# Kernel optimization log

Measured on AMD Instinct MI355X. Metric: run time of the kernel, lower is better.

The kernel has to match this reference:

```python
import jax, jax.numpy as jnp
import numpy as np

N_HEADS = 16


def setup_inputs() -> dict:
    key = jax.random.key(0)
    ks = jax.random.split(key, 6)
    B, S, E = 2, 2048, 1024
    scale = 1.0 / np.sqrt(E)
    return {
        "X": jax.random.normal(ks[0], (B, S, E), dtype=jnp.float32),
        "Wq": jax.random.normal(ks[1], (E, E), dtype=jnp.float32) * scale,
        "Wk": jax.random.normal(ks[2], (E, E), dtype=jnp.float32) * scale,
        "Wv": jax.random.normal(ks[3], (E, E), dtype=jnp.float32) * scale,
        "Wp": jax.random.normal(ks[4], (E, E), dtype=jnp.float32) * scale,
        "bp": jnp.zeros((E,), dtype=jnp.float32),
    }


def reference(X, Wq, Wk, Wv, Wp, bp):
    B, S, E = X.shape
    H = N_HEADS
    dk = E // H
    # qkv projections (Linear with weight [out,in] -> x @ W.T), split heads
    q = (X @ Wq.T).reshape(B, S, H, dk).transpose(0, 2, 1, 3)  # [B,H,S,dk]
    k = (X @ Wk.T).reshape(B, S, H, dk).transpose(0, 2, 1, 3)
    v = (X @ Wv.T).reshape(B, S, H, dk).transpose(0, 2, 1, 3)
    scores = jnp.einsum('bhqd,bhkd->bhqk', q, k) / jnp.sqrt(jnp.asarray(dk, X.dtype))
    causal = jnp.tril(jnp.ones((S, S), dtype=bool))  # [S,S]
    scores = jnp.where(causal[None, None], scores, jnp.asarray(-jnp.inf, X.dtype))
    attn = jax.nn.softmax(scores, axis=-1)  # [B,H,S,S]
    y = jnp.einsum('bhqk,bhkd->bhqd', attn, v)  # [B,H,S,dk]
    y = y.transpose(0, 2, 1, 3).reshape(B, S, E)
    return y @ Wp.T + bp
```

## Files before the change

### kernel.cpp

```cpp
#include <hip/hip_runtime.h>

typedef unsigned short u16;
typedef __bf16 bf16x8 __attribute__((ext_vector_type(8)));
typedef float f32x4 __attribute__((ext_vector_type(4)));
typedef unsigned short u16x8 __attribute__((ext_vector_type(8)));
typedef unsigned short u16x4 __attribute__((ext_vector_type(4)));

union B8 { u16x8 u; bf16x8 b; };

#define MFMA_BF16(a, b, c) __builtin_amdgcn_mfma_f32_16x16x32_bf16((a), (b), (c), 0, 0, 0)

__device__ __forceinline__ u16 f2bf(float f) {
  unsigned x = __float_as_uint(f);
  unsigned r = x + 0x7fffu + ((x >> 16) & 1u);
  return (u16)(r >> 16);
}

__device__ __forceinline__ unsigned cvt_pk_bf16(float lo, float hi) {
  unsigned r;
  asm("v_cvt_pk_bf16_f32 %0, %1, %2" : "=v"(r) : "v"(lo), "v"(hi));
  return r;
}

__device__ __forceinline__ void gl2lds16(const void* g, void* l) {
  __builtin_amdgcn_global_load_lds(
      (const __attribute__((address_space(1))) void*)g,
      (__attribute__((address_space(3))) void*)l, 16, 0, 0);
}

__global__ __launch_bounds__(256) void cast5_kernel(
    const float* __restrict__ X, const float* __restrict__ Wq,
    const float* __restrict__ Wk, const float* __restrict__ Wv,
    const float* __restrict__ Wp, u16* __restrict__ Xb, u16* __restrict__ Wqb,
    u16* __restrict__ Wkb, u16* __restrict__ Wvb, u16* __restrict__ Wpb) {
  size_t i = ((size_t)blockIdx.x * 256 + threadIdx.x) * 4;
  const float* src;
  u16* dst;
  size_t off;
  if (i < 4194304) {
    src = X; dst = Xb; off = i;
  } else if (i < 5242880) {
    src = Wq; dst = Wqb; off = i - 4194304;
  } else if (i < 6291456) {
    src = Wk; dst = Wkb; off = i - 5242880;
  } else if (i < 7340032) {
    src = Wv; dst = Wvb; off = i - 6291456;
  } else {
    src = Wp; dst = Wpb; off = i - 7340032;
  }
  float4 v = *(const float4*)(src + off);
  u16x4 o;
  o[0] = f2bf(v.x); o[1] = f2bf(v.y); o[2] = f2bf(v.z); o[3] = f2bf(v.w);
  *(u16x4*)(dst + off) = o;
}

template <int MLO>
__device__ __forceinline__ void mfma12(f32x4 (&acc)[8][3], B8 (&af)[8], B8& b0,
                                       B8& b1, B8& b2) {
  __builtin_amdgcn_s_setprio(1);
#pragma unroll
  for (int m = MLO; m < MLO + 4; ++m) {
    acc[m][0] = MFMA_BF16(af[m].b, b0.b, acc[m][0]);
    acc[m][1] = MFMA_BF16(af[m].b, b1.b, acc[m][1]);
    acc[m][2] = MFMA_BF16(af[m].b, b2.b, acc[m][2]);
  }
  __builtin_amdgcn_s_setprio(0);
}

__global__ __launch_bounds__(512, 1) void gemm_qkv192(
    const u16* __restrict__ Xb, const u16* __restrict__ Wb,
    u16* __restrict__ Qb, u16* __restrict__ Kb, u16* __restrict__ Vt) {
  __shared__ __align__(16) u16 Al[2][2][256 * 32];
  __shared__ __align__(16) u16 Bl[2][2][192 * 32];

  int tid = threadIdx.x, lane = tid & 63, w = tid >> 6;
  int wr = w >> 2, wc = w & 3;
  int l16 = lane & 15, lg = lane >> 4;

  int bid = blockIdx.x;
  int swz = (bid & 7) * 32 + (bid >> 3);
  int bm = swz >> 4, bn = swz & 15;

  const u16* Ag = Xb + (size_t)bm * 256 * 1024;
  const u16* Bg = Wb + (size_t)bn * 192 * 1024;

  int lr = lane >> 2;
  int lc = lane & 3;

  auto stA = [&](int buf, int kh, int kt) {
#pragma unroll
    for (int p2 = 0; p2 < 2; ++p2) {
      int r = p2 * 128 + w * 16 + lr;
      int sl = lc ^ ((r >> 1) & 3);
      gl2lds16(Ag + (size_t)r * 1024 + kt * 64 + kh * 32 + sl * 8,
               (char*)&Al[buf][kh][0] + (size_t)(p2 * 128 + w * 16) * 64);
    }
  };
  auto stB = [&](int buf, int kh, int kt) {
    {
      int r = w * 16 + lr;
      int sl = lc ^ ((r >> 1) & 3);
      gl2lds16(Bg + (size_t)r * 1024 + kt * 64 + kh * 32 + sl * 8,
               (char*)&Bl[buf][kh][0] + (size_t)(w * 16) * 64);
    }
    if (w < 4) {
      int r = 128 + w * 16 + lr;
      int sl = lc ^ ((r >> 1) & 3);
      gl2lds16(Bg + (size_t)r * 1024 + kt * 64 + kh * 32 + sl * 8,
               (char*)&Bl[buf][kh][0] + (size_t)(128 + w * 16) * 64);
    }
  };
  auto ldA = [&](int buf, int kk, B8 (&af)[8]) {
#pragma unroll
    for (int m = 0; m < 8; ++m) {
      int r = wr * 128 + m * 16 + l16;
      af[m].u = *(const u16x8*)((const char*)&Al[buf][kk][0] + r * 64 +
                                ((lg ^ ((r >> 1) & 3)) << 4));
    }
  };
  auto ldB = [&](int buf, int kk, int nf, B8& bf) {
    int r = wc * 48 + nf * 16 + l16;
    bf.u = *(const u16x8*)((const char*)&Bl[buf][kk][0] + r * 64 +
                           ((lg ^ ((r >> 1) & 3)) << 4));
  };

#define WAITC(LAST)                                                            \
  do {                                                                         \
    if (LAST) asm volatile("s_waitcnt vmcnt(0)" ::: "memory");                 \
    else if (w < 4) asm volatile("s_waitcnt vmcnt(8)" ::: "memory");           \
    else asm volatile("s_waitcnt vmcnt(6)" ::: "memory");                      \
  } while (0)

  f32x4 acc[8][3] = {};

  stA(0, 0, 0); stB(0, 0, 0);
  stA(0, 1, 0); stB(0, 1, 0);
  stA(1, 0, 1); stB(1, 0, 1);
  WAITC(false);
  __builtin_amdgcn_s_barrier();

  B8 af[8], b0, b1, b2;
  for (int I = 0; I < 8; ++I) {
    int p = 2 * I;
    bool last = (I == 7);
    stA(1, 1, p + 1);
    ldA(0, 0, af); ldB(0, 0, 0, b0); ldB(0, 0, 1, b1); ldB(0, 0, 2, b2);
    mfma12<0>(acc, af, b0, b1, b2);
    stB(1, 1, p + 1);
    mfma12<4>(acc, af, b0, b1, b2);
    WAITC(last);
    __builtin_amdgcn_s_barrier();
    if (!last) stA(0, 0, p + 2);
    ldA(0, 1, af); ldB(0, 1, 0, b0); ldB(0, 1, 1, b1); ldB(0, 1, 2, b2);
    mfma12<0>(acc, af, b0, b1, b2);
    if (!last) stB(0, 0, p + 2);
    mfma12<4>(acc, af, b0, b1, b2);
    WAITC(last);
    __builtin_amdgcn_s_barrier();
    if (!last) stA(0, 1, p + 2);
    ldA(1, 0, af); ldB(1, 0, 0, b0); ldB(1, 0, 1, b1); ldB(1, 0, 2, b2);
    mfma12<0>(acc, af, b0, b1, b2);
    if (!last) stB(0, 1, p + 2);
    mfma12<4>(acc, af, b0, b1, b2);
    WAITC(last);
    __builtin_amdgcn_s_barrier();
    if (!last) stA(1, 0, p + 3);
    ldA(1, 1, af); ldB(1, 1, 0, b0); ldB(1, 1, 1, b1); ldB(1, 1, 2, b2);
    mfma12<0>(acc, af, b0, b1, b2);
    if (!last) stB(1, 0, p + 3);
    mfma12<4>(acc, af, b0, b1, b2);
    if (!last) {
      WAITC(false);
      __builtin_amdgcn_s_barrier();
    }
  }
#undef WAITC

  const float QSCALE = 0.18033688011112042f;
#pragma unroll
  for (int m = 0; m < 8; ++m)
#pragma unroll
    for (int nf = 0; nf < 3; ++nf) {
      int colg = bn * 192 + wc * 48 + nf * 16 + l16;
      int rowg = bm * 256 + wr * 128 + m * 16 + lg * 4;
      if (colg < 1024) {
#pragma unroll
        for (int j = 0; j < 4; ++j)
          Qb[(size_t)(rowg + j) * 1024 + colg] = f2bf(acc[m][nf][j] * QSCALE);
      } else if (colg < 2048) {
#pragma unroll
        for (int j = 0; j < 4; ++j)
          Kb[(size_t)(rowg + j) * 1024 + (colg - 1024)] = f2bf(acc[m][nf][j]);
      } else {
        int cv = colg - 2048;
        int hh = cv >> 6, d = cv & 63;
        int bb = rowg >> 11, s0r = rowg & 2047;
        u16x4 pk;
#pragma unroll
        for (int j = 0; j < 4; ++j) pk[j] = f2bf(acc[m][nf][j]);
        *(u16x4*)(Vt + ((size_t)(bb * 16 + hh) * 64 + d) * 2048 + s0r) = pk;
      }
    }
}

__global__ __launch_bounds__(256) void gemm_proj_kernel(
    const u16* __restrict__ Y1, const u16* __restrict__ Wpb,
    float* __restrict__ out, const float* __restrict__ bias) {
  __shared__ __align__(16) u16 Asm[2][128 * 64];
  __shared__ __align__(16) u16 Bsm[2][128 * 64];

  const int Kd = 1024, N = 1024;
  int bm = blockIdx.y, bn = blockIdx.x;
  int tid = threadIdx.x;
  int lane = tid & 63, w = tid >> 6;
  int wr = w >> 1, wc = w & 1;
  int l16 = lane & 15, lg = lane >> 4;

  const u16* Abase = Y1 + (size_t)bm * 128 * Kd;
  const u16* Bbase = Wpb + (size_t)bn * 128 * Kd;

  int r0 = tid >> 3;

  auto stage = [&](int buf, int kt) {
#pragma unroll
    for (int i = 0; i < 4; ++i) {
      int r = i * 32 + r0;
      int sl = (tid & 7) ^ (r & 7);
      gl2lds16(Abase + (size_t)r * Kd + kt * 64 + sl * 8,
               &Asm[buf][i * 2048 + w * 512]);
      gl2lds16(Bbase + (size_t)r * Kd + kt * 64 + sl * 8,
               &Bsm[buf][i * 2048 + w * 512]);
    }
  };

  f32x4 acc[4][4] = {};
  stage(0, 0);
  int buf = 0;

  for (int kt = 0; kt < 16; ++kt) {
    asm volatile("s_waitcnt vmcnt(0)" ::: "memory");
    __syncthreads();
    if (kt + 1 < 16) stage(buf ^ 1, kt + 1);

    B8 af[4][2], bfr[4][2];
#pragma unroll
    for (int mi = 0; mi < 4; ++mi)
#pragma unroll
      for (int kk = 0; kk < 2; ++kk) {
        int r = wr * 64 + mi * 16 + l16;
        int s = kk * 4 + lg;
        af[mi][kk].u = *(const u16x8*)((const char*)&Asm[buf][0] + r * 128 +
                                       ((s ^ (r & 7)) << 4));
      }
#pragma unroll
    for (int ni = 0; ni < 4; ++ni)
#pragma unroll
      for (int kk = 0; kk < 2; ++kk) {
        int r = wc * 64 + ni * 16 + l16;
        int s = kk * 4 + lg;
        bfr[ni][kk].u = *(const u16x8*)((const char*)&Bsm[buf][0] + r * 128 +
                                        ((s ^ (r & 7)) << 4));
      }
    __builtin_amdgcn_s_setprio(1);
#pragma unroll
    for (int mi = 0; mi < 4; ++mi)
#pragma unroll
      for (int ni = 0; ni < 4; ++ni) {
        acc[mi][ni] = MFMA_BF16(af[mi][0].b, bfr[ni][0].b, acc[mi][ni]);
        acc[mi][ni] = MFMA_BF16(af[mi][1].b, bfr[ni][1].b, acc[mi][ni]);
      }
    __builtin_amdgcn_s_setprio(0);
    buf ^= 1;
  }

#pragma unroll
  for (int mi = 0; mi < 4; ++mi)
#pragma unroll
    for (int ni = 0; ni < 4; ++ni) {
      int col = bn * 128 + wc * 64 + ni * 16 + l16;
#pragma unroll
      for (int j = 0; j < 4; ++j) {
        int row = bm * 128 + wr * 64 + mi * 16 + lg * 4 + j;
        out[(size_t)row * N + col] = acc[mi][ni][j] + bias[col];
      }
    }
}

__global__ __launch_bounds__(256, 4) void attn_kernel(const u16* __restrict__ Q,
                                                      const u16* __restrict__ K,
                                                      const u16* __restrict__ Vt,
                                                      u16* __restrict__ Y) {
  __shared__ __align__(16) u16 Kl[2][64 * 64];
  __shared__ __align__(16) u16 Vl[2][64 * 64];
  __shared__ __align__(16) u16 Pl[4][16 * 64];

  const int E = 1024, S = 2048;
  int tid = threadIdx.x;
  int lane = tid & 63, w = tid >> 6;
  int l16 = lane & 15, lg = lane >> 4;
  int h7 = l16 & 7;

  int bid = blockIdx.x;
  int bh = bid & 31;
  int u = bid >> 5;
  int g = u & 7, kq = u >> 3;
  int qt = (kq == 0) ? 31 - g : (kq == 1) ? 16 + g : (kq == 2) ? 15 - g : g;
  int b = bh >> 4, h = bh & 15;

  const u16* Qb = Q + (size_t)b * S * E + (size_t)h * 64;
  const u16* Kb = K + (size_t)b * S * E + (size_t)h * 64;
  const u16* Vb = Vt + (size_t)bh * 64 * 2048;

  int r0 = tid >> 3;
  int s0 = (tid & 7) ^ (r0 & 7);
  size_t koff = (size_t)r0 * 1024 + s0 * 8;
  size_t voff = (size_t)r0 * 2048 + s0 * 8;
  const u16* kpA = Kb;
  const u16* kpB = Kb + 32 * 1024;
  const u16* vpA = Vb;
  const u16* vpB = Vb + 32 * 2048;

  const char* kbase0 = (const char*)&Kl[0][0] + l16 * 128 + ((lg ^ h7) << 4);
  const char* kbase1 = (const char*)&Kl[0][0] + l16 * 128 + (((4 + lg) ^ h7) << 4);
  const char* vbase0 = (const char*)&Vl[0][0] + l16 * 128 + ((lg ^ h7) << 4);
  const char* vbase1 = (const char*)&Vl[0][0] + l16 * 128 + (((4 + lg) ^ h7) << 4);
  char* pw0 = (char*)&Pl[w][0] + l16 * 128 + (((0 * 2 + (lg >> 1)) ^ h7) << 4) + (lg & 1) * 8;
  char* pw1 = (char*)&Pl[w][0] + l16 * 128 + (((1 * 2 + (lg >> 1)) ^ h7) << 4) + (lg & 1) * 8;
  char* pw2 = (char*)&Pl[w][0] + l16 * 128 + (((2 * 2 + (lg >> 1)) ^ h7) << 4) + (lg & 1) * 8;
  char* pw3 = (char*)&Pl[w][0] + l16 * 128 + (((3 * 2 + (lg >> 1)) ^ h7) << 4) + (lg & 1) * 8;
  const char* pr0 = (const char*)&Pl[w][0] + l16 * 128 + ((lg ^ h7) << 4);
  const char* pr1 = (const char*)&Pl[w][0] + l16 * 128 + (((4 + lg) ^ h7) << 4);

  B8 qa[2];
#pragma unroll
  for (int kk = 0; kk < 2; ++kk)
    qa[kk].u = *(const u16x8*)(Qb + (size_t)(qt * 64 + w * 16 + l16) * E + kk * 32 + lg * 8);

  f32x4 o[4] = {};
  float lrun = 0.f;
  int qrow = w * 16 + l16;

  gl2lds16(kpA + koff, &Kl[0][w * 512]);
  gl2lds16(vpA + voff, &Vl[0][w * 512]);
  gl2lds16(kpB + koff, &Kl[0][2048 + w * 512]);
  gl2lds16(vpB + voff, &Vl[0][2048 + w * 512]);
  kpA += 65536; kpB += 65536; vpA += 64; vpB += 64;

#define ATTN_ITER(BF, DOMASK, DOSTAGE)                                         \
  do {                                                                         \
    asm volatile("s_waitcnt vmcnt(0)" ::: "memory");                           \
    __syncthreads();                                                           \
    if (DOSTAGE) {                                                             \
      gl2lds16(kpA + koff, &Kl[(BF) ^ 1][w * 512]);                            \
      gl2lds16(vpA + voff, &Vl[(BF) ^ 1][w * 512]);                            \
      gl2lds16(kpB + koff, &Kl[(BF) ^ 1][2048 + w * 512]);                     \
      gl2lds16(vpB + voff, &Vl[(BF) ^ 1][2048 + w * 512]);                     \
      kpA += 65536; kpB += 65536; vpA += 64; vpB += 64;                        \
    }                                                                          \
    f32x4 sa[4] = {};                                                          \
    __builtin_amdgcn_s_setprio(1);                                             \
    _Pragma("unroll") for (int nb = 0; nb < 4; ++nb) {                         \
      B8 kf0, kf1;                                                             \
      kf0.u = *(const u16x8*)(kbase0 + (BF)*8192 + nb * 2048);                 \
      kf1.u = *(const u16x8*)(kbase1 + (BF)*8192 + nb * 2048);                 \
      sa[nb] = MFMA_BF16(kf0.b, qa[0].b, sa[nb]);                              \
      sa[nb] = MFMA_BF16(kf1.b, qa[1].b, sa[nb]);                              \
    }                                                                          \
    __builtin_amdgcn_s_setprio(0);                                             \
    float p[16];                                                               \
    _Pragma("unroll") for (int nb = 0; nb < 4; ++nb)                           \
        _Pragma("unroll") for (int j = 0; j < 4; ++j) {                        \
      float pe = __builtin_amdgcn_exp2f(sa[nb][j]);                            \
      if (DOMASK) {                                                            \
        int kv = nb * 16 + lg * 4 + j;                                         \
        if (kv > qrow) pe = 0.f;                                               \
      }                                                                        \
      p[nb * 4 + j] = pe;                                                      \
    }                                                                          \
    {                                                                          \
      union { u16x4 v; unsigned uu[2]; } pk;                                   \
      pk.uu[0] = cvt_pk_bf16(p[0], p[1]);                                      \
      pk.uu[1] = cvt_pk_bf16(p[2], p[3]);                                      \
      *(u16x4*)pw0 = pk.v;                                                     \
      pk.uu[0] = cvt_pk_bf16(p[4], p[5]);                                      \
      pk.uu[1] = cvt_pk_bf16(p[6], p[7]);                                      \
      *(u16x4*)pw1 = pk.v;                                                     \
      pk.uu[0] = cvt_pk_bf16(p[8], p[9]);                                      \
      pk.uu[1] = cvt_pk_bf16(p[10], p[11]);                                    \
      *(u16x4*)pw2 = pk.v;                                                     \
      pk.uu[0] = cvt_pk_bf16(p[12], p[13]);                                    \
      pk.uu[1] = cvt_pk_bf16(p[14], p[15]);                                    \
      *(u16x4*)pw3 = pk.v;                                                     \
    }                                                                          \
    lrun += ((p[0] + p[1]) + (p[2] + p[3])) + ((p[4] + p[5]) + (p[6] + p[7])) +\
            ((p[8] + p[9]) + (p[10] + p[11])) +                                \
            ((p[12] + p[13]) + (p[14] + p[15]));                               \
    B8 pa0, pa1;                                                               \
    pa0.u = *(const u16x8*)pr0;                                                \
    pa1.u = *(const u16x8*)pr1;                                                \
    __builtin_amdgcn_s_setprio(1);                                             \
    _Pragma("unroll") for (int nb = 0; nb < 4; ++nb) {                         \
      B8 vf0, vf1;                                                             \
      vf0.u = *(const u16x8*)(vbase0 + (BF)*8192 + nb * 2048);                 \
      vf1.u = *(const u16x8*)(vbase1 + (BF)*8192 + nb * 2048);                 \
      o[nb] = MFMA_BF16(pa0.b, vf0.b, o[nb]);                                  \
      o[nb] = MFMA_BF16(pa1.b, vf1.b, o[nb]);                                  \
    }                                                                          \
    __builtin_amdgcn_s_setprio(0);                                             \
  } while (0)

  int U = qt;
  int i = 0;
  for (; i + 2 <= U; i += 2) {
    ATTN_ITER(0, false, true);
    ATTN_ITER(1, false, true);
  }
  if (U & 1) {
    ATTN_ITER(0, false, true);
    ATTN_ITER(1, true, false);
  } else {
    ATTN_ITER(0, true, false);
  }
#undef ATTN_ITER

  lrun += __shfl_xor(lrun, 16);
  lrun += __shfl_xor(lrun, 32);
  float inv[4];
#pragma unroll
  for (int j = 0; j < 4; ++j) {
    float lj = __shfl(lrun, (lane & 48) | (lg * 4 + j));
    inv[j] = 1.0f / lj;
  }
#pragma unroll
  for (int nb = 0; nb < 4; ++nb)
#pragma unroll
    for (int j = 0; j < 4; ++j) {
      int row = qt * 64 + w * 16 + lg * 4 + j;
      int col = h * 64 + nb * 16 + l16;
      Y[((size_t)b * S + row) * E + col] = f2bf(o[nb][j] * inv[j]);
    }
}

extern "C" void kernel_launch(void* const* d_in, const int* in_sizes, int n_in,
                              void* d_out, int out_size, void* d_ws,
                              size_t ws_size, hipStream_t stream) {
  const float* X = (const float*)d_in[0];
  const float* Wq = (const float*)d_in[1];
  const float* Wk = (const float*)d_in[2];
  const float* Wv = (const float*)d_in[3];
  const float* Wp = (const float*)d_in[4];
  const float* bp = (const float*)d_in[5];
  float* out = (float*)d_out;

  char* ws = (char*)d_ws;
  const size_t MB = 1ull << 20;
  u16* Xb = (u16*)(ws + 0 * MB);
  u16* Wqb = (u16*)(ws + 8 * MB);
  u16* Wkb = (u16*)(ws + 10 * MB);
  u16* Wvb = (u16*)(ws + 12 * MB);
  u16* Wpb = (u16*)(ws + 14 * MB);
  u16* Qb = (u16*)(ws + 16 * MB);
  u16* Kb = (u16*)(ws + 24 * MB);
  u16* VtB = (u16*)(ws + 32 * MB);
  u16* Y1 = (u16*)(ws + 40 * MB);

  cast5_kernel<<<8192, 256, 0, stream>>>(X, Wq, Wk, Wv, Wp, Xb, Wqb, Wkb, Wvb, Wpb);
  gemm_qkv192<<<256, 512, 0, stream>>>(Xb, Wqb, Qb, Kb, VtB);
  attn_kernel<<<1024, 256, 0, stream>>>(Qb, Kb, VtB, Y1);
  gemm_proj_kernel<<<dim3(8, 32), 256, 0, stream>>>(Y1, Wpb, out, bp);
}
```

Before: 104.8 us.

## Split softmax P into halves to overlap with PV MFMA; row sums via MFMA

The attention inner loop now computes exp and the bf16 pack for the first half of the score tile, issues its PV MFMAs, then handles the second half. This interleaves transcendental work with matrix-core work. The softmax row sum is computed by an extra MFMA of P against a ones vector instead of scalar adds and end-of-loop shuffles. This adds two extra MFMAs, LDS waits and sched barriers per iteration. It also changes the denominator to use the bf16-rounded P values, which makes it consistent with the numerator.

New measurement: 105.8 us. About the same (+1.0%).

```diff
diff --git a/kernel.cpp b/kernel.cpp
--- a/kernel.cpp
+++ b/kernel.cpp
@@ -336,8 +336,12 @@
   for (int kk = 0; kk < 2; ++kk)
     qa[kk].u = *(const u16x8*)(Qb + (size_t)(qt * 64 + w * 16 + l16) * E + kk * 32 + lg * 8);
 
+  B8 ones;
+#pragma unroll
+  for (int j = 0; j < 8; ++j) ones.u[j] = 0x3F80;
+
   f32x4 o[4] = {};
-  float lrun = 0.f;
+  f32x4 lsv = {};
   int qrow = w * 16 + l16;
 
   gl2lds16(kpA + koff, &Kl[0][w * 512]);
@@ -367,43 +371,67 @@
       sa[nb] = MFMA_BF16(kf1.b, qa[1].b, sa[nb]);                              \
     }                                                                          \
     __builtin_amdgcn_s_setprio(0);                                             \
-    float p[16];                                                               \
-    _Pragma("unroll") for (int nb = 0; nb < 4; ++nb)                           \
+                                                \
+    float p0[8];                                                               \
+    _Pragma("unroll") for (int nb = 0; nb < 2; ++nb)                           \
         _Pragma("unroll") for (int j = 0; j < 4; ++j) {                        \
       float pe = __builtin_amdgcn_exp2f(sa[nb][j]);                            \
       if (DOMASK) {                                                            \
         int kv = nb * 16 + lg * 4 + j;                                         \
         if (kv > qrow) pe = 0.f;                                               \
       }                                                                        \
-      p[nb * 4 + j] = pe;                                                      \
+      p0[nb * 4 + j] = pe;                                                     \
     }                                                                          \
     {                                                                          \
       union { u16x4 v; unsigned uu[2]; } pk;                                   \
-      pk.uu[0] = cvt_pk_bf16(p[0], p[1]);                                      \
-      pk.uu[1] = cvt_pk_bf16(p[2], p[3]);                                      \
+      pk.uu[0] = cvt_pk_bf16(p0[0], p0[1]);                                    \
+      pk.uu[1] = cvt_pk_bf16(p0[2], p0[3]);                                    \
       *(u16x4*)pw0 = pk.v;                                                     \
-      pk.uu[0] = cvt_pk_bf16(p[4], p[5]);                                      \
-      pk.uu[1] = cvt_pk_bf16(p[6], p[7]);                                      \
+      pk.uu[0] = cvt_pk_bf16(p0[4], p0[5]);                                    \
+      pk.uu[1] = cvt_pk_bf16(p0[6], p0[7]);                                    \
       *(u16x4*)pw1 = pk.v;                                                     \
-      pk.uu[0] = cvt_pk_bf16(p[8], p[9]);                                      \
-      pk.uu[1] = cvt_pk_bf16(p[10], p[11]);                                    \
+    }                                                                          \
+    asm volatile("s_waitcnt lgkmcnt(0)" ::: "memory");                         \
+    __builtin_amdgcn_sched_barrier(0);                                         \
+    B8 pa0;                                                                    \
+    pa0.u = *(const u16x8*)pr0;                                                \
+    __builtin_amdgcn_s_setprio(1);                                             \
+    lsv = MFMA_BF16(pa0.b, ones.b, lsv);                                       \
+    _Pragma("unroll") for (int nb = 0; nb < 4; ++nb) {                         \
+      B8 vf0;                                                                  \
+      vf0.u = *(const u16x8*)(vbase0 + (BF)*8192 + nb * 2048);                 \
+      o[nb] = MFMA_BF16(pa0.b, vf0.b, o[nb]);                                  \
+    }                                                                          \
+    __builtin_amdgcn_s_setprio(0);                                             \
+             \
+    float p1[8];                                                               \
+    _Pragma("unroll") for (int nb = 2; nb < 4; ++nb)                           \
+        _Pragma("unroll") for (int j = 0; j < 4; ++j) {                        \
+      float pe = __builtin_amdgcn_exp2f(sa[nb][j]);                            \
+      if (DOMASK) {                                                            \
+        int kv = nb * 16 + lg * 4 + j;                                         \
+        if (kv > qrow) pe = 0.f;                                               \
+      }                                                                        \
+      p1[(nb - 2) * 4 + j] = pe;                                               \
+    }                                                                          \
+    {                                                                          \
+      union { u16x4 v; unsigned uu[2]; } pk;                                   \
+      pk.uu[0] = cvt_pk_bf16(p1[0], p1[1]);                                    \
+      pk.uu[1] = cvt_pk_bf16(p1[2], p1[3]);                                    \
       *(u16x4*)pw2 = pk.v;                                                     \
-      pk.uu[0] = cvt_pk_bf16(p[12], p[13]);                                    \
-      pk.uu[1] = cvt_pk_bf16(p[14], p[15]);                                    \
+      pk.uu[0] = cvt_pk_bf16(p1[4], p1[5]);                                    \
+      pk.uu[1] = cvt_pk_bf16(p1[6], p1[7]);                                    \
       *(u16x4*)pw3 = pk.v;                                                     \
     }                                                                          \
-    lrun += ((p[0] + p[1]) + (p[2] + p[3])) + ((p[4] + p[5]) + (p[6] + p[7])) +\
-            ((p[8] + p[9]) + (p[10] + p[11])) +                                \
-            ((p[12] + p[13]) + (p[14] + p[15]));                               \
-    B8 pa0, pa1;                                                               \
-    pa0.u = *(const u16x8*)pr0;                                                \
+    asm volatile("s_waitcnt lgkmcnt(0)" ::: "memory");                         \
+    __builtin_amdgcn_sched_barrier(0);                                         \
+    B8 pa1;                                                                    \
     pa1.u = *(const u16x8*)pr1;                                                \
     __builtin_amdgcn_s_setprio(1);                                             \
+    lsv = MFMA_BF16(pa1.b, ones.b, lsv);                                       \
     _Pragma("unroll") for (int nb = 0; nb < 4; ++nb) {                         \
-      B8 vf0, vf1;                                                             \
-      vf0.u = *(const u16x8*)(vbase0 + (BF)*8192 + nb * 2048);                 \
+      B8 vf1;                                                                  \
       vf1.u = *(const u16x8*)(vbase1 + (BF)*8192 + nb * 2048);                 \
-      o[nb] = MFMA_BF16(pa0.b, vf0.b, o[nb]);                                  \
       o[nb] = MFMA_BF16(pa1.b, vf1.b, o[nb]);                                  \
     }                                                                          \
     __builtin_amdgcn_s_setprio(0);                                             \
@@ -423,14 +451,9 @@
   }
 #undef ATTN_ITER
 
-  lrun += __shfl_xor(lrun, 16);
-  lrun += __shfl_xor(lrun, 32);
   float inv[4];
 #pragma unroll
-  for (int j = 0; j < 4; ++j) {
-    float lj = __shfl(lrun, (lane & 48) | (lg * 4 + j));
-    inv[j] = 1.0f / lj;
-  }
+  for (int j = 0; j < 4; ++j) inv[j] = 1.0f / lsv[j];
 #pragma unroll
   for (int nb = 0; nb < 4; ++nb)
 #pragma unroll
```
